# Optimization experiments

Measured on AMD Instinct MI355X. Metric: run time of the kernel, lower is better.

## Reference

```python
import jax, jax.numpy as jnp
import numpy as np

HOP = jnp.array([0, 1, 4, 7, 2, 5, 8, 3, 6, 9, 11, 14, 10, 12, 15, 13, 16])
GRAPH = jnp.array([0, 1, 4, 7, 2, 5, 8, 3, 6, 9, 12, 10, 13, 15, 11, 14, 16])
D_MODEL, L, D_INNER, D_STATE, DT_RANK = 512, 17, 1024, 4, 32


def layernorm(x, w, b, eps=1e-5):
    mu = x.mean(-1, keepdims=True)
    var = ((x - mu) ** 2).mean(-1, keepdims=True)
    return (x - mu) * jax.lax.rsqrt(var + eps) * w + b


def setup_inputs() -> dict:
    key = jax.random.key(0)
    ks = jax.random.split(key, 9)
    B = 4096
    s = lambda k, shape: jax.random.normal(k, shape, jnp.float32) * 0.02
    # A_log init per mamba_ssm: log(1..d_state) repeated over d_inner
    A_log = jnp.log(jnp.broadcast_to(jnp.arange(1, D_STATE + 1, dtype=jnp.float32), (D_INNER, D_STATE)))
    return {
        "x": jax.random.normal(ks[0], (B, L, D_MODEL), jnp.float32),
        "bp_embed": s(ks[1], (1, 5, D_MODEL)),
        "ln_w": jnp.ones((D_MODEL,), jnp.float32),
        "ln_b": jnp.zeros((D_MODEL,), jnp.float32),
        "in_proj_w": s(ks[2], (2 * D_INNER, D_MODEL)),
        "conv_w": 1.0 + s(ks[3], (D_INNER,)),  # d_conv=1 depthwise conv == per-channel scale
        "conv_b": jnp.zeros((D_INNER,), jnp.float32),
        "x_proj_w": s(ks[4], (DT_RANK + 2 * D_STATE, D_INNER)),
        "dt_proj_w": s(ks[5], (D_INNER, DT_RANK)),
        "dt_proj_b": s(ks[6], (D_INNER,)) - 4.0,  # softplus-inverse-ish small dt init
        "A_log": A_log,
        "D": jnp.ones((D_INNER,), jnp.float32),
        "out_proj_w": s(ks[7], (D_MODEL, D_INNER)),
    }


def mamba(u, in_proj_w, conv_w, conv_b, x_proj_w, dt_proj_w, dt_proj_b, A_log, D, out_proj_w):
    # u: [B, L, d_model]
    xz = jnp.einsum('bld,ed->ble', u, in_proj_w)          # [B,L,2*d_inner]
    xm, z = jnp.split(xz, 2, axis=-1)
    xm = jax.nn.silu(xm * conv_w + conv_b)                 # d_conv=1 -> pointwise
    x_dbl = jnp.einsum('ble,fe->blf', xm, x_proj_w)        # [B,L,dt_rank+2*d_state]
    dt_r = x_dbl[..., :DT_RANK]
    Bm = x_dbl[..., DT_RANK:DT_RANK + D_STATE]
    Cm = x_dbl[..., DT_RANK + D_STATE:]
    dt = jax.nn.softplus(jnp.einsum('blr,er->ble', dt_r, dt_proj_w) + dt_proj_b)  # [B,L,d_inner]
    A = -jnp.exp(A_log)                                    # [d_inner,d_state]

    def step(h, inp):
        dt_t, B_t, C_t, x_t = inp                          # [B,di],[B,ds],[B,ds],[B,di]
        dA = jnp.exp(dt_t[..., None] * A)                  # [B,di,ds]
        h = dA * h + (dt_t * x_t)[..., None] * B_t[:, None, :]
        y = jnp.einsum('bes,bs->be', h, C_t)
        return h, y

    bsz = u.shape[0]
    h0 = jnp.zeros((bsz, D_INNER, D_STATE), u.dtype)
    seq = (dt.transpose(1, 0, 2), Bm.transpose(1, 0, 2), Cm.transpose(1, 0, 2), xm.transpose(1, 0, 2))
    _, ys = jax.lax.scan(step, h0, seq)                    # ys: [L,B,d_inner]
    y = ys.transpose(1, 0, 2) + xm * D
    y = y * jax.nn.silu(z)
    return jnp.einsum('ble,de->bld', y, out_proj_w)


def reference(x, bp_embed, ln_w, ln_b, in_proj_w, conv_w, conv_b, x_proj_w,
              dt_proj_w, dt_proj_b, A_log, D, out_proj_w):
    bp = bp_embed
    x_bpe = jnp.concatenate([bp[:, :3], bp[:, :3], bp[:, :3], bp[:, :1],
                             bp[:, 3:], bp[:, :1], bp[:, 3:], bp[:, 3:]], axis=1)  # [1,17,dim]
    x_ssm = x[:, HOP, :] + x_bpe
    x_ssm = layernorm(x_ssm, ln_w, ln_b)
    x_ssm = mamba(x_ssm, in_proj_w, conv_w, conv_b, x_proj_w,
                  dt_proj_w, dt_proj_b, A_log, D, out_proj_w)
    return x + x_ssm[:, GRAPH, :]
```

## Files before the change

### kernel.cpp

```cpp
#include <hip/hip_runtime.h>

typedef unsigned short u16;
typedef unsigned int   u32;
typedef __bf16 bf16_t;
typedef bf16_t bf16x8 __attribute__((ext_vector_type(8)));
typedef float  f32x4  __attribute__((ext_vector_type(4)));

#define DEV static __device__ __forceinline__

__constant__ int c_HOP[17] = {0,1,4,7,2,5,8,3,6,9,11,14,10,12,15,13,16};
__constant__ int c_BPE[17] = {0,1,2,0,1,2,0,1,2,0,3,4,0,3,4,3,4};

DEV u16 f2bf(float f){
  u32 x = __builtin_bit_cast(u32, f);
  x += 0x7fffu + ((x >> 16) & 1u);
  return (u16)(x >> 16);
}
DEV float bf2f(u32 u){ return __builtin_bit_cast(float, u << 16); }
DEV float silu_f(float v){ return v / (1.f + __expf(-v)); }
DEV float softplus_f(float s){ return (s > 20.f) ? s : log1pf(__expf(s)); }

DEV void gll16(const void* g, void* l){
  __builtin_amdgcn_global_load_lds((__attribute__((address_space(1))) void*)g,
                                   (__attribute__((address_space(3))) void*)l,
                                   16, 0, 0);
}

__global__ __launch_bounds__(256) void cvt4(
    const float* __restrict__ s0, u16* __restrict__ d0, int n0,
    const float* __restrict__ s1, u16* __restrict__ d1, int n1,
    const float* __restrict__ s2, u16* __restrict__ d2, int n2,
    const float* __restrict__ s3, u16* __restrict__ d3, int n3)
{
  int t = blockIdx.x * 256 + threadIdx.x;
  if (t < n0){ d0[t] = f2bf(s0[t]); return; }
  t -= n0; if (t < n1){ d1[t] = f2bf(s1[t]); return; }
  t -= n1; if (t < n2){ d2[t] = f2bf(s2[t]); return; }
  t -= n2; if (t < n3){ d3[t] = f2bf(s3[t]); }
}

__global__ __launch_bounds__(256) void ln_gather(
    const float* __restrict__ x, const float* __restrict__ bpe,
    const float* __restrict__ lnw, const float* __restrict__ lnb,
    u16* __restrict__ u)
{
  int tok = blockIdx.x;
  int b = tok / 17;
  int l = tok - b * 17;
  const float* xr = x   + ((size_t)b * 17 + c_HOP[l]) * 512;
  const float* br = bpe + (size_t)c_BPE[l] * 512;
  int tid = threadIdx.x;
  int d0 = tid * 2;
  float2 xv = *(const float2*)(xr + d0);
  float2 bv = *(const float2*)(br + d0);
  float v0 = xv.x + bv.x, v1 = xv.y + bv.y;

  __shared__ float red[8];
  float s = v0 + v1;
  #pragma unroll
  for (int o = 32; o; o >>= 1) s += __shfl_xor(s, o);
  if ((tid & 63) == 0) red[tid >> 6] = s;
  __syncthreads();
  float mu = (red[0] + red[1] + red[2] + red[3]) * (1.f / 512.f);
  float a0 = v0 - mu, a1 = v1 - mu;
  float q = a0 * a0 + a1 * a1;
  #pragma unroll
  for (int o = 32; o; o >>= 1) q += __shfl_xor(q, o);
  if ((tid & 63) == 0) red[4 + (tid >> 6)] = q;
  __syncthreads();
  float var = (red[4] + red[5] + red[6] + red[7]) * (1.f / 512.f);
  float rs = rsqrtf(var + 1e-5f);

  u16 o0 = f2bf(a0 * rs * lnw[d0]     + lnb[d0]);
  u16 o1 = f2bf(a1 * rs * lnw[d0 + 1] + lnb[d0 + 1]);
  u32 pack = (u32)o0 | ((u32)o1 << 16);
  *(u32*)(u + (size_t)tok * 512 + d0) = pack;
}

enum { EPI_SPLIT = 0, EPI_OUT = 1, EPI_XDBL = 2, EPI_DT = 3 };

template<int EPI>
__global__ __launch_bounds__(512, 2) void gemm256(
    const u16* __restrict__ A, int lda,
    const u16* __restrict__ W, int K, int MT,
    u16* __restrict__ ob0, u16* __restrict__ ob1,
    const float* __restrict__ p0, const float* __restrict__ p1,
    const float* __restrict__ xres, float* __restrict__ fout)
{
  __shared__ u16 sA[2][2][8192];
  __shared__ u16 sB[2][2][8192];

  int nwg = gridDim.x;
  int cpx = nwg >> 3;
  int wg = (blockIdx.x & 7) * cpx + (blockIdx.x >> 3);
  int NT = nwg / MT;
  int nt = wg % NT, mt = wg / NT;
  int brow = mt * 256, bcol = nt * 256;
  int tid = threadIdx.x, lane = tid & 63, wid = tid >> 6;
  int wm = wid >> 2, wn = wid & 3;
  int l15 = lane & 15, lhi = lane >> 4;

  f32x4 acc[8][4] = {};

  int sr0 = tid >> 2, sr1 = 128 + (tid >> 2), sch = tid & 3;
  const u16* gA0 = A + (size_t)(brow + sr0) * lda + (sch ^ ((sr0 >> 1) & 3)) * 8;
  const u16* gA1 = A + (size_t)(brow + sr1) * lda + (sch ^ ((sr1 >> 1) & 3)) * 8;
  const u16* gW0 = W + (size_t)(bcol + sr0) * K   + (sch ^ ((sr0 >> 1) & 3)) * 8;
  const u16* gW1 = W + (size_t)(bcol + sr1) * K   + (sch ^ ((sr1 >> 1) & 3)) * 8;

  auto stA = [&](int buf, int kh, int koff) {
    char* d = (char*)&sA[buf][kh][0] + tid * 16;
    gll16(gA0 + koff, d);
    gll16(gA1 + koff, d + 8192);
  };
  auto stB = [&](int buf, int kh, int koff) {
    char* d = (char*)&sB[buf][kh][0] + tid * 16;
    gll16(gW0 + koff, d);
    gll16(gW1 + koff, d + 8192);
  };

  int aoff[2][4], boff[4];
  #pragma unroll
  for (int mh = 0; mh < 2; mh++)
    #pragma unroll
    for (int mi = 0; mi < 4; mi++) {
      int r = wm * 128 + mh * 64 + mi * 16 + l15;
      aoff[mh][mi] = r * 64 + ((lhi ^ ((r >> 1) & 3)) * 16);
    }
  #pragma unroll
  for (int ni = 0; ni < 4; ni++) {
    int r = wn * 64 + ni * 16 + l15;
    boff[ni] = r * 64 + ((lhi ^ ((r >> 1) & 3)) * 16);
  }

  bf16x8 bvv[4];

#define PHASE(buf, kh, MH, RB)                                              \
  {                                                                         \
    const char* la = (const char*)&sA[buf][kh][0];                          \
    bf16x8 av0 = *(const bf16x8*)(la + aoff[MH][0]);                        \
    bf16x8 av1 = *(const bf16x8*)(la + aoff[MH][1]);                        \
    bf16x8 av2 = *(const bf16x8*)(la + aoff[MH][2]);                        \
    bf16x8 av3 = *(const bf16x8*)(la + aoff[MH][3]);                        \
    if (RB) {                                                               \
      const char* lb = (const char*)&sB[buf][kh][0];                        \
      bvv[0] = *(const bf16x8*)(lb + boff[0]);                              \
      bvv[1] = *(const bf16x8*)(lb + boff[1]);                              \
      bvv[2] = *(const bf16x8*)(lb + boff[2]);                              \
      bvv[3] = *(const bf16x8*)(lb + boff[3]);                              \
    }                                                                       \
    __builtin_amdgcn_s_setprio(1);                                          \
    _Pragma("unroll")                                                       \
    for (int ni = 0; ni < 4; ni++) {                                        \
      acc[(MH)*4+0][ni] = __builtin_amdgcn_mfma_f32_16x16x32_bf16(av0, bvv[ni], acc[(MH)*4+0][ni], 0,0,0); \
      acc[(MH)*4+1][ni] = __builtin_amdgcn_mfma_f32_16x16x32_bf16(av1, bvv[ni], acc[(MH)*4+1][ni], 0,0,0); \
      acc[(MH)*4+2][ni] = __builtin_amdgcn_mfma_f32_16x16x32_bf16(av2, bvv[ni], acc[(MH)*4+2][ni], 0,0,0); \
      acc[(MH)*4+3][ni] = __builtin_amdgcn_mfma_f32_16x16x32_bf16(av3, bvv[ni], acc[(MH)*4+3][ni], 0,0,0); \
    }                                                                       \
    __builtin_amdgcn_s_setprio(0);                                          \
  }

#define WAITBAR                                                             \
  asm volatile("s_waitcnt vmcnt(4)" ::: "memory");                          \
  __builtin_amdgcn_s_barrier();                                             \
  __builtin_amdgcn_sched_barrier(0);

  int T = K >> 6;
  stA(0, 0, 0); stB(0, 0, 0);
  stA(0, 1, 32); stB(0, 1, 32);
  WAITBAR;

  for (int t = 0; t < T; ++t) {
    int b = t & 1;
    int nk = (t + 1) << 6;
    bool pf = (t + 1 < T);
    if (pf) stA(b ^ 1, 0, nk);
    PHASE(b, 0, 0, true);
    if (pf) stB(b ^ 1, 0, nk);
    PHASE(b, 0, 1, false);
    WAITBAR;
    if (pf) stA(b ^ 1, 1, nk + 32);
    PHASE(b, 1, 0, true);
    if (pf) stB(b ^ 1, 1, nk + 32);
    PHASE(b, 1, 1, false);
    WAITBAR;
  }
#undef PHASE
#undef WAITBAR

  int r4 = lhi * 4;
  #pragma unroll
  for (int fm = 0; fm < 8; fm++) {
    int rowb = brow + wm * 128 + fm * 16 + r4;
    #pragma unroll
    for (int ni = 0; ni < 4; ni++) {
      int col = bcol + wn * 64 + ni * 16 + l15;
      if constexpr (EPI == EPI_SPLIT) {
        bool isx = (bcol < 1024);
        int cidx = isx ? col : 0;
        float cw = isx ? p0[cidx] : 1.f;
        float cb = isx ? p1[cidx] : 0.f;
        u16* dst = isx ? (ob0 + col) : (ob1 + col - 1024);
        #pragma unroll
        for (int rr = 0; rr < 4; rr++)
          dst[(size_t)(rowb + rr) * 1024] = f2bf(silu_f(acc[fm][ni][rr] * cw + cb));
      } else {
        #pragma unroll
        for (int rr = 0; rr < 4; rr++) {
          int row = rowb + rr;
          u32 rw = (u32)row;
          u32 b = rw / 17u;
          int gl = (int)(rw - b * 17u);
          size_t oi = ((size_t)b * 17 + c_HOP[gl]) * 512 + col;
          fout[oi] = xres[oi] + acc[fm][ni][rr];
        }
      }
    }
  }
}

template<int EPI>
__global__ __launch_bounds__(256) void gemm_bt(
    const u16* __restrict__ A, int lda,
    const u16* __restrict__ W, int K, int MT,
    u16* __restrict__ ob0, const float* __restrict__ p0)
{
  __shared__ u16 sA[2][128 * 32];
  __shared__ u16 sW[2][128 * 32];
  int nwg = gridDim.x;
  int cpx = nwg >> 3;
  int wg = (blockIdx.x & 7) * cpx + (blockIdx.x >> 3);
  int NT = nwg / MT;
  int nt = wg % NT, mt = wg / NT;
  int brow = mt * 128, bcol = nt * 128;
  int tid = threadIdx.x, lane = tid & 63, wid = tid >> 6;
  int wm = wid >> 1, wn = wid & 1;

  f32x4 acc[4][4] = {};

  int srow = tid >> 2;
  int sch  = tid & 3;

  const u16* gA0 = A + (size_t)(brow + srow)      * lda + (sch ^ ((srow >> 1) & 3)) * 8;
  const u16* gA1 = A + (size_t)(brow + 64 + srow) * lda + (sch ^ (((64 + srow) >> 1) & 3)) * 8;
  const u16* gW0 = W + (size_t)(bcol + srow)      * K   + (sch ^ ((srow >> 1) & 3)) * 8;
  const u16* gW1 = W + (size_t)(bcol + 64 + srow) * K   + (sch ^ (((64 + srow) >> 1) & 3)) * 8;

  auto STAGE = [&](int buf, int kt) {
    gll16(gA0 + kt, (char*)sA[buf] + tid * 16);
    gll16(gA1 + kt, (char*)sA[buf] + tid * 16 + 4096);
    gll16(gW0 + kt, (char*)sW[buf] + tid * 16);
    gll16(gW1 + kt, (char*)sW[buf] + tid * 16 + 4096);
  };

  int aoff[4], boff[4];
  #pragma unroll
  for (int mi = 0; mi < 4; mi++) {
    int r = wm * 64 + mi * 16 + (lane & 15);
    aoff[mi] = r * 64 + (((lane >> 4) ^ ((r >> 1) & 3)) * 16);
  }
  #pragma unroll
  for (int ni = 0; ni < 4; ni++) {
    int r = wn * 64 + ni * 16 + (lane & 15);
    boff[ni] = r * 64 + (((lane >> 4) ^ ((r >> 1) & 3)) * 16);
  }

  auto COMPUTE = [&](int buf) {
    bf16x8 av[4], bv[4];
    #pragma unroll
    for (int mi = 0; mi < 4; mi++)
      av[mi] = *(const bf16x8*)((const char*)sA[buf] + aoff[mi]);
    #pragma unroll
    for (int ni = 0; ni < 4; ni++)
      bv[ni] = *(const bf16x8*)((const char*)sW[buf] + boff[ni]);
    #pragma unroll
    for (int mi = 0; mi < 4; mi++)
      #pragma unroll
      for (int ni = 0; ni < 4; ni++)
        acc[mi][ni] = __builtin_amdgcn_mfma_f32_16x16x32_bf16(
            av[mi], bv[ni], acc[mi][ni], 0, 0, 0);
  };

  int nsteps = K >> 5;
  STAGE(0, 0);
  __syncthreads();
  int cur = 0;
  for (int s = 1; s < nsteps; ++s) {
    STAGE(cur ^ 1, s << 5);
    COMPUTE(cur);
    __syncthreads();
    cur ^= 1;
  }
  COMPUTE(cur);

  int r4 = (lane >> 4) * 4;
  int cl = lane & 15;
  #pragma unroll
  for (int mi = 0; mi < 4; mi++) {
    int rowb = brow + wm * 64 + mi * 16 + r4;
    #pragma unroll
    for (int ni = 0; ni < 4; ni++) {
      int col = bcol + wn * 64 + ni * 16 + cl;
      if constexpr (EPI == EPI_XDBL) {
        if (col < 40) {
          #pragma unroll
          for (int rr = 0; rr < 4; rr++)
            ob0[(size_t)(rowb + rr) * 40 + col] = f2bf(acc[mi][ni][rr]);
        }
      } else {
        float bb = p0[col];
        #pragma unroll
        for (int rr = 0; rr < 4; rr++)
          ob0[(size_t)(rowb + rr) * 1024 + col] = f2bf(softplus_f(acc[mi][ni][rr] + bb));
      }
    }
  }
}

__global__ __launch_bounds__(128) void scan5(
    const u16* __restrict__ xm, const u16* __restrict__ zs,
    const u16* __restrict__ xdbl, u16* __restrict__ dty,
    const float* __restrict__ A_log, const float* __restrict__ Dp)
{
  int b = blockIdx.x;
  int tid = threadIdx.x;
  int e0 = tid * 8;
  const size_t base = (size_t)b * 17 * 1024;

  float4 al = *(const float4*)(A_log + (size_t)e0 * 4);
  float A0 = -__expf(al.x), A1 = -__expf(al.y);
  float A2 = -__expf(al.z), A3 = -__expf(al.w);
  float Dv[8];
  *(float4*)(Dv)     = *(const float4*)(Dp + e0);
  *(float4*)(Dv + 4) = *(const float4*)(Dp + e0 + 4);

  const u16* xmb = xm + base + e0;
  const u16* zsb = zs + base + e0;
  u16* db = dty + base + e0;
  const u16* bcb = xdbl + (size_t)b * 680 + 32;

  float h[8][4];
  #pragma unroll
  for (int c = 0; c < 8; c++)
    #pragma unroll
    for (int s = 0; s < 4; s++) h[c][s] = 0.f;

  #pragma unroll
  for (int t = 0; t < 17; t++) {
    uint4 xr = *(const uint4*)(xmb + t * 1024);
    uint4 zr = *(const uint4*)(zsb + t * 1024);
    uint4 dr = *(const uint4*)(db + t * 1024);
    uint4 bc = *(const uint4*)(bcb + t * 40);
    float B0 = bf2f(bc.x & 0xffffu), B1 = bf2f(bc.x >> 16);
    float B2 = bf2f(bc.y & 0xffffu), B3 = bf2f(bc.y >> 16);
    float C0 = bf2f(bc.z & 0xffffu), C1 = bf2f(bc.z >> 16);
    float C2 = bf2f(bc.w & 0xffffu), C3 = bf2f(bc.w >> 16);
    u32 yo[4];
    const u32* xw = (const u32*)&xr;
    const u32* zw = (const u32*)&zr;
    const u32* dw = (const u32*)&dr;
    #pragma unroll
    for (int c = 0; c < 8; c++) {
      u32 x16 = (c & 1) ? (xw[c >> 1] >> 16) : (xw[c >> 1] & 0xffffu);
      u32 z16 = (c & 1) ? (zw[c >> 1] >> 16) : (zw[c >> 1] & 0xffffu);
      u32 d16 = (c & 1) ? (dw[c >> 1] >> 16) : (dw[c >> 1] & 0xffffu);
      float xv = bf2f(x16), zv = bf2f(z16), dtv = bf2f(d16);
      float dx = dtv * xv;
      h[c][0] = __expf(dtv * A0) * h[c][0] + dx * B0;
      h[c][1] = __expf(dtv * A1) * h[c][1] + dx * B1;
      h[c][2] = __expf(dtv * A2) * h[c][2] + dx * B2;
      h[c][3] = __expf(dtv * A3) * h[c][3] + dx * B3;
      float yv = h[c][0] * C0 + h[c][1] * C1 + h[c][2] * C2 + h[c][3] * C3;
      u16 pk = f2bf((yv + xv * Dv[c]) * zv);
      if (c & 1) yo[c >> 1] |= ((u32)pk << 16);
      else       yo[c >> 1] = (u32)pk;
    }
    *(uint4*)(db + t * 1024) = *(uint4*)yo;
  }
}

extern "C" void kernel_launch(void* const* d_in, const int* in_sizes, int n_in,
                              void* d_out, int out_size, void* d_ws, size_t ws_size,
                              hipStream_t stream) {
  const float* x     = (const float*)d_in[0];
  const float* bpe   = (const float*)d_in[1];
  const float* lnw   = (const float*)d_in[2];
  const float* lnb   = (const float*)d_in[3];
  const float* w_in  = (const float*)d_in[4];
  const float* convw = (const float*)d_in[5];
  const float* convb = (const float*)d_in[6];
  const float* w_xp  = (const float*)d_in[7];
  const float* w_dt  = (const float*)d_in[8];
  const float* b_dt  = (const float*)d_in[9];
  const float* A_log = (const float*)d_in[10];
  const float* Dp    = (const float*)d_in[11];
  const float* w_out = (const float*)d_in[12];
  float* out = (float*)d_out;

  u16* ws = (u16*)d_ws;
  u16* wb_in  = ws;
  u16* wb_out = wb_in  + 1048576;
  u16* wb_xp  = wb_out + 524288;
  u16* wb_dt  = wb_xp  + 40960;
  u16* xm     = wb_dt  + 32768;
  u16* zs     = xm     + 71303168;
  u16* xdbl   = zs     + 71303168;
  u16* dty    = xdbl   + 2785280;
  u16* u      = dty;

  const int MT2 = 272;
  const int MT1 = 544;

  cvt4<<<6432, 256, 0, stream>>>(w_in, wb_in, 1048576, w_out, wb_out, 524288,
                                 w_xp, wb_xp, 40960, w_dt, wb_dt, 32768);

  ln_gather<<<69632, 256, 0, stream>>>(x, bpe, lnw, lnb, u);

  gemm256<EPI_SPLIT><<<MT2 * 8, 512, 0, stream>>>(
      u, 512, wb_in, 512, MT2, xm, zs, convw, convb, nullptr, nullptr);

  gemm_bt<EPI_XDBL><<<MT1 * 1, 256, 0, stream>>>(
      xm, 1024, wb_xp, 1024, MT1, xdbl, nullptr);

  gemm_bt<EPI_DT><<<MT1 * 8, 256, 0, stream>>>(
      xdbl, 40, wb_dt, 32, MT1, dty, b_dt);

  scan5<<<4096, 128, 0, stream>>>(xm, zs, xdbl, dty, A_log, Dp);

  gemm256<EPI_OUT><<<MT2 * 2, 512, 0, stream>>>(
      dty, 1024, wb_out, 1024, MT2, nullptr, nullptr, nullptr, nullptr, x, out);
}
```

Measured before the change: 894.6 us.

## Deepen GEMM LDS prefetch pipeline with half-tile granularity and extra barriers

Restructures the main GEMM K-loop so global-to-LDS loads are issued one and a half tiles ahead, in half-tile stages, instead of one tile ahead. Each phase issues its stage load after reading LDS fragments and then hits a barrier before the MFMA block, and vmcnt waits are adjusted to keep 8 loads in flight. The goal is to hide global load latency better. In exchange there are more barriers per iteration and the buffer-reuse timing is more delicate.

```diff
diff --git a/kernel.cpp b/kernel.cpp
--- a/kernel.cpp
+++ b/kernel.cpp
@@ -135,7 +135,7 @@
 
   bf16x8 bvv[4];
 
-#define PHASE(buf, kh, MH, RB)                                              \
+#define PH(buf, kh, MH, RB, STAGE)                                          \
   {                                                                         \
     const char* la = (const char*)&sA[buf][kh][0];                          \
     bf16x8 av0 = *(const bf16x8*)(la + aoff[MH][0]);                        \
@@ -149,6 +149,9 @@
       bvv[2] = *(const bf16x8*)(lb + boff[2]);                              \
       bvv[3] = *(const bf16x8*)(lb + boff[3]);                              \
     }                                                                       \
+    STAGE                                                                   \
+    __builtin_amdgcn_s_barrier();                                           \
+    __builtin_amdgcn_sched_barrier(0);                                      \
     __builtin_amdgcn_s_setprio(1);                                          \
     _Pragma("unroll")                                                       \
     for (int ni = 0; ni < 4; ni++) {                                        \
@@ -160,33 +163,34 @@
     __builtin_amdgcn_s_setprio(0);                                          \
   }
 
-#define WAITBAR                                                             \
-  asm volatile("s_waitcnt vmcnt(4)" ::: "memory");                          \
-  __builtin_amdgcn_s_barrier();                                             \
-  __builtin_amdgcn_sched_barrier(0);
-
   int T = K >> 6;
-  stA(0, 0, 0); stB(0, 0, 0);
+
+  stA(0, 0, 0);  stB(0, 0, 0);
   stA(0, 1, 32); stB(0, 1, 32);
-  WAITBAR;
+  stA(1, 0, 64); stB(1, 0, 64);
+  asm volatile("s_waitcnt vmcnt(8)" ::: "memory");
+  __builtin_amdgcn_s_barrier();
 
   for (int t = 0; t < T; ++t) {
     int b = t & 1;
-    int nk = (t + 1) << 6;
-    bool pf = (t + 1 < T);
-    if (pf) stA(b ^ 1, 0, nk);
-    PHASE(b, 0, 0, true);
-    if (pf) stB(b ^ 1, 0, nk);
-    PHASE(b, 0, 1, false);
-    WAITBAR;
-    if (pf) stA(b ^ 1, 1, nk + 32);
-    PHASE(b, 1, 0, true);
-    if (pf) stB(b ^ 1, 1, nk + 32);
-    PHASE(b, 1, 1, false);
-    WAITBAR;
-  }
-#undef PHASE
-#undef WAITBAR
+    bool s1 = (t + 1 < T), s2 = (t + 2 < T);
+    int k1off = ((t + 1) << 6) + 32;
+    int k2off = (t + 2) << 6;
+
+    PH(b, 0, 0, true,  { if (s1) stA(b ^ 1, 1, k1off); });
+    __builtin_amdgcn_s_barrier();
+    PH(b, 0, 1, false, { if (s1) stB(b ^ 1, 1, k1off); });
+    if (t < T - 1) { asm volatile("s_waitcnt vmcnt(8)" ::: "memory"); }
+    else           { asm volatile("s_waitcnt vmcnt(0)" ::: "memory"); }
+    __builtin_amdgcn_s_barrier();
+    PH(b, 1, 0, true,  { if (s2) stA(b, 0, k2off); });
+    __builtin_amdgcn_s_barrier();
+    PH(b, 1, 1, false, { if (s2) stB(b, 0, k2off); });
+    if (t < T - 2)       { asm volatile("s_waitcnt vmcnt(8)" ::: "memory"); }
+    else if (t == T - 2) { asm volatile("s_waitcnt vmcnt(4)" ::: "memory"); }
+    __builtin_amdgcn_s_barrier();
+  }
+#undef PH
 
   int r4 = lhi * 4;
   #pragma unroll
```

Result: faster. 872.0 us (-2.5%).
